# Optimization experiments

Measured on AMD Instinct MI355X. Metric: run time of the kernel, lower is better.

The kernel has to match this reference:

```python
import jax, jax.numpy as jnp
import numpy as np

DIM = 1536
DEPTH = 8
HEADS = 8
KV_HEADS = 1
GROUPS = HEADS // KV_HEADS
DQK = 128
DV = 192
DIM_PW = 128
POOL = 16
FF_INNER = int(DIM * 2.0)
SOFTCLAMP = 5.0
SCALE = 64 ** -0.5  # source uses default dim_head=64 for scale, not dim_head_qk
MAX_POS = 8192
EPS = float(jnp.finfo(jnp.float32).eps)


def rmsnorm(x, g):
    return x * jax.lax.rsqrt(jnp.mean(x * x, axis=-1, keepdims=True) + EPS) * g


def rotate_half(x):
    x1, x2 = jnp.split(x, 2, axis=-1)
    return jnp.concatenate([-x2, x1], axis=-1)


def apply_rope(pos, t):
    return t * jnp.cos(pos) + rotate_half(t) * jnp.sin(pos)


def rotary_emb(seq_len):
    nf = DQK // 2
    # torch.logspace(1, MAX_POS-nf+1, nf) = 10**linspace -> overflows to inf in fp32 (faithful)
    inv_freq = 1.0 / (jnp.arange(nf, dtype=jnp.float32) + 10.0 ** jnp.linspace(1.0, MAX_POS - nf + 1, nf, dtype=jnp.float32))
    freqs = jnp.arange(seq_len, dtype=jnp.float32)[:, None] * inv_freq[None, :]
    return jnp.concatenate([freqs, freqs], axis=-1)  # [n, DQK]


def softclamp(t, value=SOFTCLAMP):
    return jnp.tanh(t / value) * value


def attention(x, pairwise, rope, w_qkv, qg, kg, vg, bg, w_bias, w_out):
    b, n, _ = x.shape
    qkv = x @ w_qkv
    q, k, v = jnp.split(qkv, [HEADS * DQK, HEADS * DQK + DQK], axis=-1)
    # b n (g h d) -> b g h n d
    q = q.reshape(b, n, GROUPS, KV_HEADS, DQK).transpose(0, 2, 3, 1, 4)
    k = k.reshape(b, n, KV_HEADS, DQK).transpose(0, 2, 1, 3)
    v = v.reshape(b, n, KV_HEADS, DV).transpose(0, 2, 1, 3)
    q = rmsnorm(q, qg)
    k = rmsnorm(k, kg)
    v = rmsnorm(v, vg)
    q = q * SCALE
    q = apply_rope(rope, q)
    k = apply_rope(rope, k)
    sim = jnp.einsum('bghid,bhjd->bghij', q, k)
    # pairwise bias: RMSNorm -> GELU -> Linear(dim_pw, heads) -> b g h i j
    pb = jax.nn.gelu(rmsnorm(pairwise, bg), approximate=False) @ w_bias  # [b, i, j, heads]
    bi = pb.shape[1]
    bias = pb.reshape(b, bi, bi, GROUPS, KV_HEADS).transpose(0, 3, 4, 1, 2)
    bias = jnp.repeat(jnp.repeat(bias, POOL, axis=3), POOL, axis=4)  # expand to seq res
    sim = softclamp(sim + bias)
    attn = jax.nn.softmax(sim, axis=-1)
    out = jnp.einsum('bghij,bhjd->bghid', attn, v)
    out = out.transpose(0, 3, 1, 2, 4).reshape(b, n, GROUPS * KV_HEADS * DV)
    return out @ w_out


def tower(x, pairwise, w_qkv, q_gamma, k_gamma, v_gamma, bias_gamma, w_bias, w_out, attn_pre_gamma, ff_pre_gamma, w_ff1, b_ff1, w_ff2, b_ff2):
    rope = rotary_emb(x.shape[1])
    for d in range(DEPTH):
        xn = rmsnorm(x, attn_pre_gamma[d])
        x = x + attention(xn, pairwise, rope, w_qkv[d], q_gamma[d], k_gamma[d], v_gamma[d], bias_gamma[d], w_bias[d], w_out[d])
        xn = rmsnorm(x, ff_pre_gamma[d])
        x = x + (jax.nn.relu(xn @ w_ff1[d] + b_ff1[d]) @ w_ff2[d] + b_ff2[d])
    return x


def setup_inputs() -> dict:
    key = jax.random.key(0)
    ks = jax.random.split(key, 10)
    s = 0.02
    inp = {
        'x': jax.random.normal(ks[0], (2, 2048, DIM), jnp.float32),
        'pairwise': jax.random.normal(ks[1], (2, 128, 128, DIM_PW), jnp.float32),
        'w_qkv': jax.random.normal(ks[2], (DEPTH, DIM, HEADS * DQK + DQK + DV), jnp.float32) * s,
        'q_gamma': jnp.ones((DEPTH, DQK), jnp.float32),
        'k_gamma': jnp.ones((DEPTH, DQK), jnp.float32),
        'v_gamma': jnp.ones((DEPTH, DV), jnp.float32),
        'bias_gamma': jnp.ones((DEPTH, DIM_PW), jnp.float32),
        'w_bias': jax.random.normal(ks[3], (DEPTH, DIM_PW, HEADS), jnp.float32) * s,
        'w_out': jax.random.normal(ks[4], (DEPTH, DV * HEADS, DIM), jnp.float32) * s,
        'attn_pre_gamma': jnp.ones((DEPTH, DIM), jnp.float32),
        'ff_pre_gamma': jnp.ones((DEPTH, DIM), jnp.float32),
        'w_ff1': jax.random.normal(ks[5], (DEPTH, DIM, FF_INNER), jnp.float32) * s,
        'b_ff1': jnp.zeros((DEPTH, FF_INNER), jnp.float32),
        'w_ff2': jax.random.normal(ks[6], (DEPTH, FF_INNER, DIM), jnp.float32) * s,
        'b_ff2': jnp.zeros((DEPTH, DIM), jnp.float32),
    }
    return inp


def reference(x, pairwise, w_qkv, q_gamma, k_gamma, v_gamma, bias_gamma, w_bias, w_out, attn_pre_gamma, ff_pre_gamma, w_ff1, b_ff1, w_ff2, b_ff2):
    return tower(x, pairwise, w_qkv, q_gamma, k_gamma, v_gamma, bias_gamma, w_bias, w_out, attn_pre_gamma, ff_pre_gamma, w_ff1, b_ff1, w_ff2, b_ff2)
```

## Files before the change

### kernel.cpp

```cpp
#include <hip/hip_runtime.h>

typedef __bf16 bf16;
typedef float f32x4 __attribute__((ext_vector_type(4)));
typedef __bf16 bf16x8 __attribute__((ext_vector_type(8)));
typedef __bf16 bf16x4 __attribute__((ext_vector_type(4)));

#define EPSF 1.1920928955078125e-07f

#define GLOAD_LDS16(gsrc, ldst) \
  __builtin_amdgcn_global_load_lds((const __attribute__((address_space(1))) void*)(gsrc), \
                                   (__attribute__((address_space(3))) void*)(ldst), 16, 0, 0)

__device__ __forceinline__ float wave_reduce_sum(float v) {
#pragma unroll
  for (int m = 1; m < 64; m <<= 1) v += __shfl_xor(v, m, 64);
  return v;
}

__global__ __launch_bounds__(256) void wcast_t(const float* __restrict__ src,
                                               bf16* __restrict__ dst, int R, int C) {
  __shared__ float t[32][33];
  int z = blockIdx.z;
  const float* s = src + (size_t)z * R * C;
  bf16* d = dst + (size_t)z * R * C;
  int c0 = blockIdx.x * 32, r0 = blockIdx.y * 32;
  int tx = threadIdx.x, ty = threadIdx.y;
#pragma unroll
  for (int k = 0; k < 4; ++k)
    t[ty + k * 8][tx] = s[(size_t)(r0 + ty + k * 8) * C + c0 + tx];
  __syncthreads();
#pragma unroll
  for (int k = 0; k < 4; ++k)
    d[(size_t)(c0 + ty + k * 8) * R + r0 + tx] = (bf16)t[tx][ty + k * 8];
}

__global__ __launch_bounds__(256) void rmsnorm_k(const float* __restrict__ X,
                                                 const float* __restrict__ G,
                                                 bf16* __restrict__ O) {
  int row = blockIdx.x, tid = threadIdx.x, lane = tid & 63, w = tid >> 6;
  const float* x = X + (size_t)row * 1536;
  float v[6];
  float ss = 0.f;
#pragma unroll
  for (int k = 0; k < 6; ++k) { v[k] = x[tid + k * 256]; ss += v[k] * v[k]; }
  ss = wave_reduce_sum(ss);
  __shared__ float wsum[4];
  if (lane == 0) wsum[w] = ss;
  __syncthreads();
  ss = wsum[0] + wsum[1] + wsum[2] + wsum[3];
  float rs = rsqrtf(ss * (1.f / 1536.f) + EPSF);
  bf16* o = O + (size_t)row * 1536;
#pragma unroll
  for (int k = 0; k < 6; ++k) o[tid + k * 256] = (bf16)(v[k] * rs * G[tid + k * 256]);
}

template <int EPI>
__global__ __launch_bounds__(256, 3) void gemm_bt(const bf16* __restrict__ A,
                                                  const bf16* __restrict__ Bt,
                                                  float* __restrict__ Cf,
                                                  bf16* __restrict__ Cb,
                                                  const float* __restrict__ bias,
                                                  int M, int N, int K) {
  __shared__ __align__(16) char As[128 * 128];
  __shared__ __align__(16) char Bs[128 * 128];
  const int tid = threadIdx.x;
  const int lane = tid & 63, l15 = lane & 15, l4 = lane >> 4;
  const int w = tid >> 6;
  const int rm = blockIdx.y * 128;
  const int cn = blockIdx.x * 128;
  const int wm = (w >> 1) * 64, wn = (w & 1) * 64;
  f32x4 acc[4][4] = {};

  for (int kk = 0; kk < K; kk += 64) {
#pragma unroll
    for (int r = 0; r < 4; ++r) {
      uint32_t o = (uint32_t)(r * 256 + tid) * 16;
      uint32_t row = o >> 7;
      uint32_t kb = ((o >> 4) & 7) ^ (row & 7);
      const bf16* src = A + (size_t)(rm + (int)row) * K + kk + kb * 8;
      GLOAD_LDS16(src, As + (o & 0xFFFFFC00u));
    }
#pragma unroll
    for (int r = 0; r < 4; ++r) {
      uint32_t o = (uint32_t)(r * 256 + tid) * 16;
      uint32_t row = o >> 7;
      uint32_t kb = ((o >> 4) & 7) ^ (row & 7);
      int nrow = cn + (int)row;
      if (nrow >= N) nrow = N - 1;
      const bf16* src = Bt + (size_t)nrow * K + kk + kb * 8;
      GLOAD_LDS16(src, Bs + (o & 0xFFFFFC00u));
    }
    __syncthreads();
#pragma unroll
    for (int s = 0; s < 2; ++s) {
      bf16x8 a[4], b[4];
#pragma unroll
      for (int m = 0; m < 4; ++m) {
        uint32_t row = wm + m * 16 + l15;
        uint32_t kb = (uint32_t)(s * 4 + l4);
        a[m] = *(const bf16x8*)(As + row * 128 + (kb ^ (row & 7)) * 16);
      }
#pragma unroll
      for (int n = 0; n < 4; ++n) {
        uint32_t row = wn + n * 16 + l15;
        uint32_t kb = (uint32_t)(s * 4 + l4);
        b[n] = *(const bf16x8*)(Bs + row * 128 + (kb ^ (row & 7)) * 16);
      }
      __builtin_amdgcn_s_setprio(1);
#pragma unroll
      for (int m = 0; m < 4; ++m)
#pragma unroll
        for (int n = 0; n < 4; ++n)
          acc[m][n] = __builtin_amdgcn_mfma_f32_16x16x32_bf16(a[m], b[n], acc[m][n], 0, 0, 0);
      __builtin_amdgcn_s_setprio(0);
    }
    __syncthreads();
  }

#pragma unroll
  for (int m = 0; m < 4; ++m)
#pragma unroll
    for (int n = 0; n < 4; ++n)
#pragma unroll
      for (int r = 0; r < 4; ++r) {
        int row = rm + wm + m * 16 + l4 * 4 + r;
        int col = cn + wn + n * 16 + l15;
        if (col < N) {
          float v = acc[m][n][r];
          if constexpr (EPI == 0) {
            Cf[(size_t)row * N + col] = v;
          } else if constexpr (EPI == 2) {
            Cf[(size_t)row * N + col] += v;
          } else if constexpr (EPI == 3) {
            float tv = v + bias[col];
            Cb[(size_t)row * N + col] = (bf16)(tv > 0.f ? tv : 0.f);
          } else if constexpr (EPI == 4) {
            Cf[(size_t)row * N + col] += v + bias[col];
          }
        }
      }
}

__global__ void qkv_post(const float* __restrict__ qkv, const float* __restrict__ qg,
                         const float* __restrict__ kg, const float* __restrict__ vg,
                         bf16* __restrict__ Qo, bf16* __restrict__ Ko, bf16* __restrict__ Vo) {
  int t = blockIdx.x, seg = blockIdx.y, lane = threadIdx.x;
  int b = t >> 11, n = t & 2047;
  const float* base;
  const float* gamma;
  int len;
  if (seg < 8) { base = qkv + (size_t)t * 1344 + seg * 128; gamma = qg; len = 128; }
  else if (seg == 8) { base = qkv + (size_t)t * 1344 + 1024; gamma = kg; len = 128; }
  else { base = qkv + (size_t)t * 1344 + 1152; gamma = vg; len = 192; }
  float v0 = base[lane], v1 = base[lane + 64];
  float v2 = (len == 192) ? base[lane + 128] : 0.f;
  float ss = wave_reduce_sum(v0 * v0 + v1 * v1 + v2 * v2);
  float rs = rsqrtf(ss / (float)len + EPSF);
  float n0 = v0 * rs * gamma[lane];
  float n1 = v1 * rs * gamma[lane + 64];
  if (seg < 8) {
    n0 *= 0.125f; n1 *= 0.125f;
    if (lane == 0) {
      float th = 0.1f * (float)n;
      float c = cosf(th), s_ = sinf(th);
      float r0 = n0 * c - n1 * s_, r1 = n1 * c + n0 * s_;
      n0 = r0; n1 = r1;
    }
    bf16* q = Qo + ((size_t)((b * 8 + seg) * 2048 + n)) * 128;
    q[lane] = (bf16)n0; q[lane + 64] = (bf16)n1;
  } else if (seg == 8) {
    if (lane == 0) {
      float th = 0.1f * (float)n;
      float c = cosf(th), s_ = sinf(th);
      float r0 = n0 * c - n1 * s_, r1 = n1 * c + n0 * s_;
      n0 = r0; n1 = r1;
    }
    bf16* k = Ko + ((size_t)(b * 2048 + n)) * 128;
    k[lane] = (bf16)n0; k[lane + 64] = (bf16)n1;
  } else {
    float n2 = v2 * rs * vg[lane + 128];
    bf16* vp = Vo + ((size_t)(b * 2048 + n)) * 192;
    vp[lane] = (bf16)n0; vp[lane + 64] = (bf16)n1; vp[lane + 128] = (bf16)n2;
  }
}

__global__ __launch_bounds__(256) void vtrans(const bf16* __restrict__ V, bf16* __restrict__ Vt) {
  __shared__ bf16 t[32][33];
  int b = blockIdx.z;
  int j0 = blockIdx.x * 32, d0 = blockIdx.y * 32;
  int tx = threadIdx.x, ty = threadIdx.y;
#pragma unroll
  for (int k = 0; k < 4; ++k)
    t[ty + k * 8][tx] = V[((size_t)b * 2048 + j0 + ty + k * 8) * 192 + d0 + tx];
  __syncthreads();
#pragma unroll
  for (int k = 0; k < 4; ++k)
    Vt[((size_t)b * 192 + d0 + ty + k * 8) * 2048 + j0 + tx] = t[tx][ty + k * 8];
}

__global__ void bias_pw(const float* __restrict__ P, const float* __restrict__ g,
                        const float* __restrict__ Wb, float* __restrict__ Bout) {
  int j = blockIdx.x, i = blockIdx.y, b = blockIdx.z;
  int lane = threadIdx.x;
  const float* p = P + (((size_t)b * 128 + i) * 128 + j) * 128;
  float a0 = p[lane], a1 = p[lane + 64];
  float ss = wave_reduce_sum(a0 * a0 + a1 * a1);
  float rs = rsqrtf(ss * (1.f / 128.f) + EPSF);
  float x0 = a0 * rs * g[lane], x1 = a1 * rs * g[lane + 64];
  float g0 = 0.5f * x0 * (1.f + erff(x0 * 0.70710678118654752f));
  float g1 = 0.5f * x1 * (1.f + erff(x1 * 0.70710678118654752f));
  __shared__ float gs[128];
  gs[lane] = g0; gs[lane + 64] = g1;
  __syncthreads();
  int h = lane & 7;
  float acc = 0.f;
#pragma unroll
  for (int k = 0; k < 16; ++k) {
    int c = (lane >> 3) + k * 8;
    acc += gs[c] * Wb[c * 8 + h];
  }
  acc += __shfl_xor(acc, 8, 64);
  acc += __shfl_xor(acc, 16, 64);
  acc += __shfl_xor(acc, 32, 64);
  if (lane < 8) Bout[(((size_t)b * 8 + lane) * 128 + i) * 128 + j] = acc;
}

__global__ __launch_bounds__(256, 2) void attn_k(const bf16* __restrict__ Q,
                                                 const bf16* __restrict__ Kg,
                                                 const bf16* __restrict__ Vt,
                                                 const float* __restrict__ Bias,
                                                 bf16* __restrict__ O0, bf16* __restrict__ O1,
                                                 float* __restrict__ L0, float* __restrict__ L1) {
  __shared__ __align__(16) char Ks[64 * 256];
  __shared__ __align__(16) char Vs[192 * 128];
  __shared__ __align__(16) char Ps[128 * 128];
  __shared__ float BiasS[8 * 128];
  int tid = threadIdx.x, lane = tid & 63, w = tid >> 6;
  int it = blockIdx.x, g = blockIdx.y, bz = blockIdx.z;
  int b = bz >> 1, js = bz & 1;
  bf16* __restrict__ Op = js ? O1 : O0;
  float* __restrict__ Lp = js ? L1 : L0;
  int i0 = it * 128;
  int l15 = lane & 15, l4 = lane >> 4;

  bf16x8 qf[2][4];
#pragma unroll
  for (int m = 0; m < 2; ++m)
#pragma unroll
    for (int s = 0; s < 4; ++s)
      qf[m][s] = *(const bf16x8*)(Q + ((size_t)((b * 8 + g) * 2048 + i0 + w * 32 + m * 16 + l15)) * 128 + s * 32 + l4 * 8);

  {
    int r = tid >> 5, c = (tid & 31) * 4;
    *(float4*)&BiasS[r * 128 + c] =
        *(const float4*)(Bias + ((size_t)((b * 8 + g) * 128) + (i0 >> 4) + r) * 128 + c);
  }

  f32x4 accO[2][12] = {};
  float lacc[2] = {0.f, 0.f};

  for (int jt = js * 16; jt < js * 16 + 16; ++jt) {
    int j0 = jt * 64;
#pragma unroll
    for (int r = 0; r < 4; ++r) {
      uint32_t o = (uint32_t)(r * 256 + tid) * 16;
      uint32_t row = o >> 8;
      uint32_t kb = ((o >> 4) & 15) ^ (row & 15);
      const bf16* src = Kg + ((size_t)b * 2048 + j0 + (int)row) * 128 + kb * 8;
      GLOAD_LDS16(src, Ks + (o & 0xFFFFFC00u));
    }
#pragma unroll
    for (int r = 0; r < 6; ++r) {
      uint32_t o = (uint32_t)(r * 256 + tid) * 16;
      uint32_t dv = o >> 7;
      uint32_t kb = ((o >> 4) & 7) ^ (dv & 7);
      const bf16* src = Vt + ((size_t)b * 192 + dv) * 2048 + j0 + kb * 8;
      GLOAD_LDS16(src, Vs + (o & 0xFFFFFC00u));
    }
    __syncthreads();

    f32x4 accS[2][4] = {};
#pragma unroll
    for (int s = 0; s < 4; ++s) {
      bf16x8 kf[4];
#pragma unroll
      for (int n = 0; n < 4; ++n) {
        uint32_t row = n * 16 + l15;
        uint32_t kb = (uint32_t)(s * 4 + l4);
        kf[n] = *(const bf16x8*)(Ks + row * 256 + (kb ^ (row & 15)) * 16);
      }
      __builtin_amdgcn_s_setprio(1);
#pragma unroll
      for (int n = 0; n < 4; ++n)
#pragma unroll
        for (int m = 0; m < 2; ++m)
          accS[m][n] = __builtin_amdgcn_mfma_f32_16x16x32_bf16(kf[n], qf[m][s], accS[m][n], 0, 0, 0);
      __builtin_amdgcn_s_setprio(0);
    }

#pragma unroll
    for (int m = 0; m < 2; ++m) {
#pragma unroll
      for (int n = 0; n < 4; ++n) {
        float bia = BiasS[(w * 2 + m) * 128 + jt * 4 + n];
        bf16x4 pk;
#pragma unroll
        for (int r = 0; r < 4; ++r) {
          float sv = accS[m][n][r] + bia;
          float e1 = exp2f(0.57707801635558535f * sv);
          float th = 1.f - 2.f / (e1 + 1.f);
          float pv = exp2f(7.2134752044448170f * th);
          lacc[m] += pv;
          pk[r] = (bf16)pv;
        }
        uint32_t prow = (uint32_t)(w * 32 + m * 16 + l15);
        uint32_t byteo = prow * 128 + (uint32_t)(n * 16 + l4 * 4) * 2;
        byteo ^= (prow & 7) << 4;
        *(bf16x4*)(Ps + byteo) = pk;
      }
    }

#pragma unroll
    for (int s = 0; s < 2; ++s) {
      bf16x8 pa[2];
#pragma unroll
      for (int m = 0; m < 2; ++m) {
        uint32_t row = (uint32_t)(w * 32 + m * 16 + l15);
        uint32_t byteo = row * 128 + (uint32_t)(s * 64 + l4 * 16);
        byteo ^= (row & 7) << 4;
        pa[m] = *(const bf16x8*)(Ps + byteo);
      }
#pragma unroll
      for (int n = 0; n < 12; ++n) {
        uint32_t dvr = n * 16 + l15;
        uint32_t kb = (uint32_t)(s * 4 + l4);
        bf16x8 vf = *(const bf16x8*)(Vs + dvr * 128 + (kb ^ (dvr & 7)) * 16);
        __builtin_amdgcn_s_setprio(1);
#pragma unroll
        for (int m = 0; m < 2; ++m)
          accO[m][n] = __builtin_amdgcn_mfma_f32_16x16x32_bf16(vf, pa[m], accO[m][n], 0, 0, 0);
        __builtin_amdgcn_s_setprio(0);
      }
    }
    __syncthreads();
  }

#pragma unroll
  for (int m = 0; m < 2; ++m) {
    float l = lacc[m];
    l += __shfl_xor(l, 16, 64);
    l += __shfl_xor(l, 32, 64);
    lacc[m] = l;
  }
  if (l4 == 0) {
#pragma unroll
    for (int m = 0; m < 2; ++m)
      Lp[(size_t)(b * 8 + g) * 2048 + i0 + w * 32 + m * 16 + l15] = lacc[m];
  }

#pragma unroll
  for (int m = 0; m < 2; ++m) {
    int i = i0 + w * 32 + m * 16 + l15;
#pragma unroll
    for (int n = 0; n < 12; ++n) {
      bf16x4 ok;
#pragma unroll
      for (int r = 0; r < 4; ++r) ok[r] = (bf16)accO[m][n][r];
      int dv = n * 16 + l4 * 4;
      *(bf16x4*)(Op + ((size_t)(b * 8 + g) * 2048 + i) * 192 + dv) = ok;
    }
  }
}

__global__ __launch_bounds__(256) void attn_cmb(const bf16* __restrict__ O0,
                                                const bf16* __restrict__ O1,
                                                const float* __restrict__ L0,
                                                const float* __restrict__ L1,
                                                bf16* __restrict__ Out) {
  size_t e = ((size_t)blockIdx.x * 256u + threadIdx.x) * 8u;
  uint32_t dv = (uint32_t)(e % 192u);
  uint32_t rest = (uint32_t)(e / 192u);
  uint32_t i = rest & 2047u;
  uint32_t g = (rest >> 11) & 7u;
  uint32_t b = rest >> 14;
  bf16x8 a = *(const bf16x8*)(O0 + e);
  bf16x8 c = *(const bf16x8*)(O1 + e);
  float rl = 1.f / (L0[rest] + L1[rest]);
  bf16x8 t;
#pragma unroll
  for (int k = 0; k < 8; ++k) t[k] = (bf16)(((float)a[k] + (float)c[k]) * rl);
  *(bf16x8*)(Out + ((size_t)(b * 2048 + i)) * 1536 + g * 192 + dv) = t;
}

extern "C" void kernel_launch(void* const* d_in, const int* in_sizes, int n_in,
                              void* d_out, int out_size, void* d_ws, size_t ws_size,
                              hipStream_t stream) {
  (void)in_sizes; (void)n_in; (void)out_size;
  const float* x_in = (const float*)d_in[0];
  const float* pairwise = (const float*)d_in[1];
  const float* w_qkv = (const float*)d_in[2];
  const float* q_gamma = (const float*)d_in[3];
  const float* k_gamma = (const float*)d_in[4];
  const float* v_gamma = (const float*)d_in[5];
  const float* bias_gamma = (const float*)d_in[6];
  const float* w_bias = (const float*)d_in[7];
  const float* w_out = (const float*)d_in[8];
  const float* attn_pre = (const float*)d_in[9];
  const float* ff_pre = (const float*)d_in[10];
  const float* w_ff1 = (const float*)d_in[11];
  const float* b_ff1 = (const float*)d_in[12];
  const float* w_ff2 = (const float*)d_in[13];
  const float* b_ff2 = (const float*)d_in[14];

  char* p = (char*)d_ws;
  auto alloc = [&](size_t bytes) {
    char* r = p;
    p += (bytes + 255) & ~(size_t)255;
    return r;
  };
  bf16* wT_qkv = (bf16*)alloc(8ull * 1344 * 1536 * 2);
  bf16* wT_out = (bf16*)alloc(8ull * 1536 * 1536 * 2);
  bf16* wT_ff1 = (bf16*)alloc(8ull * 3072 * 1536 * 2);
  bf16* wT_ff2 = (bf16*)alloc(8ull * 1536 * 3072 * 2);
  float* x_ws = (float*)alloc(4096ull * 1536 * 4);
  bf16* xn = (bf16*)alloc(4096ull * 1536 * 2);
  float* qkvb = (float*)alloc(4096ull * 1344 * 4);
  bf16* qb = (bf16*)alloc(2ull * 8 * 2048 * 128 * 2);
  bf16* kb = (bf16*)alloc(2ull * 2048 * 128 * 2);
  bf16* vb = (bf16*)alloc(2ull * 2048 * 192 * 2);
  bf16* vtb = (bf16*)alloc(2ull * 192 * 2048 * 2);
  float* biasb = (float*)alloc(2ull * 8 * 128 * 128 * 4);
  bf16* attn_o = (bf16*)alloc(4096ull * 1536 * 2);
  bf16* hb = (bf16*)alloc(4096ull * 3072 * 2);
  bf16* op0 = (bf16*)alloc(2ull * 8 * 2048 * 192 * 2);
  bf16* op1 = (bf16*)alloc(2ull * 8 * 2048 * 192 * 2);
  float* lp0 = (float*)alloc(2ull * 8 * 2048 * 4);
  float* lp1 = (float*)alloc(2ull * 8 * 2048 * 4);
  if ((size_t)(p - (char*)d_ws) > ws_size) return;

  wcast_t<<<dim3(42, 48, 8), dim3(32, 8), 0, stream>>>(w_qkv, wT_qkv, 1536, 1344);
  wcast_t<<<dim3(48, 48, 8), dim3(32, 8), 0, stream>>>(w_out, wT_out, 1536, 1536);
  wcast_t<<<dim3(96, 48, 8), dim3(32, 8), 0, stream>>>(w_ff1, wT_ff1, 1536, 3072);
  wcast_t<<<dim3(48, 96, 8), dim3(32, 8), 0, stream>>>(w_ff2, wT_ff2, 3072, 1536);

  hipMemcpyAsync(x_ws, x_in, 4096ull * 1536 * 4, hipMemcpyDeviceToDevice, stream);

  for (int d = 0; d < 8; ++d) {
    const bf16* wq = wT_qkv + (size_t)d * 1344 * 1536;
    const bf16* wo = wT_out + (size_t)d * 1536 * 1536;
    const bf16* w1 = wT_ff1 + (size_t)d * 3072 * 1536;
    const bf16* w2 = wT_ff2 + (size_t)d * 1536 * 3072;

    rmsnorm_k<<<4096, 256, 0, stream>>>(x_ws, attn_pre + d * 1536, xn);
    gemm_bt<0><<<dim3(11, 32), 256, 0, stream>>>(xn, wq, qkvb, nullptr, nullptr, 4096, 1344, 1536);
    qkv_post<<<dim3(4096, 10), 64, 0, stream>>>(qkvb, q_gamma + d * 128, k_gamma + d * 128,
                                                v_gamma + d * 192, qb, kb, vb);
    vtrans<<<dim3(64, 6, 2), dim3(32, 8), 0, stream>>>(vb, vtb);
    bias_pw<<<dim3(128, 128, 2), 64, 0, stream>>>(pairwise, bias_gamma + d * 128,
                                                  w_bias + d * 128 * 8, biasb);
    attn_k<<<dim3(16, 8, 4), 256, 0, stream>>>(qb, kb, vtb, biasb, op0, op1, lp0, lp1);
    attn_cmb<<<3072, 256, 0, stream>>>(op0, op1, lp0, lp1, attn_o);
    gemm_bt<2><<<dim3(12, 32), 256, 0, stream>>>(attn_o, wo, x_ws, nullptr, nullptr, 4096, 1536, 1536);
    rmsnorm_k<<<4096, 256, 0, stream>>>(x_ws, ff_pre + d * 1536, xn);
    gemm_bt<3><<<dim3(24, 32), 256, 0, stream>>>(xn, w1, nullptr, hb, b_ff1 + d * 3072, 4096, 3072, 1536);
    gemm_bt<4><<<dim3(12, 32), 256, 0, stream>>>(hb, w2, x_ws, nullptr, b_ff2 + d * 1536, 4096, 1536, 3072);
  }

  hipMemcpyAsync(d_out, x_ws, 4096ull * 1536 * 4, hipMemcpyDeviceToDevice, stream);
}
```

Baseline: 2.876 ms.

## Split-K GEMMs with atomic accumulation, XCD block swizzle, and cheaper softclamp math

Three GEMMs now split K in two across blockIdx.z and accumulate with float atomicAdd into the output. The QKV output is zeroed first with a memset. Block IDs are remapped so consecutive tiles go to the same XCD, which targets L2 reuse. The attention kernel pre-scales the bias and rewrites the tanh-then-exp softclamp as one FMA, an exp2, a hardware reciprocal and an exp2; attn_cmb also uses the hardware reciprocal. Split-K aims to fill 256 CUs with the small grids, but it adds atomic traffic, an extra memset, and non-deterministic summation order.

```diff
diff --git a/kernel.cpp b/kernel.cpp
--- a/kernel.cpp
+++ b/kernel.cpp
@@ -54,7 +54,7 @@
   for (int k = 0; k < 6; ++k) o[tid + k * 256] = (bf16)(v[k] * rs * G[tid + k * 256]);
 }
 
-template <int EPI>
+template <int EPI, int SPLIT>
 __global__ __launch_bounds__(256, 3) void gemm_bt(const bf16* __restrict__ A,
                                                   const bf16* __restrict__ Bt,
                                                   float* __restrict__ Cf,
@@ -66,12 +66,21 @@
   const int tid = threadIdx.x;
   const int lane = tid & 63, l15 = lane & 15, l4 = lane >> 4;
   const int w = tid >> 6;
-  const int rm = blockIdx.y * 128;
-  const int cn = blockIdx.x * 128;
+  const int nwg = gridDim.x * gridDim.y;
+  const int bid = blockIdx.y * gridDim.x + blockIdx.x;
+  const int cpx = nwg >> 3;
+  const int swz = (bid & 7) * cpx + (bid >> 3);
+  const int rm = (swz / gridDim.x) * 128;
+  const int cn = (swz % gridDim.x) * 128;
   const int wm = (w >> 1) * 64, wn = (w & 1) * 64;
+  int kbeg = 0, kend = K;
+  if constexpr (SPLIT == 2) {
+    kbeg = blockIdx.z * (K >> 1);
+    kend = kbeg + (K >> 1);
+  }
   f32x4 acc[4][4] = {};
 
-  for (int kk = 0; kk < K; kk += 64) {
+  for (int kk = kbeg; kk < kend; kk += 64) {
 #pragma unroll
     for (int r = 0; r < 4; ++r) {
       uint32_t o = (uint32_t)(r * 256 + tid) * 16;
@@ -127,15 +136,21 @@
         int col = cn + wn + n * 16 + l15;
         if (col < N) {
           float v = acc[m][n][r];
+          size_t idx = (size_t)row * N + col;
           if constexpr (EPI == 0) {
-            Cf[(size_t)row * N + col] = v;
+            if constexpr (SPLIT > 1) atomicAdd(&Cf[idx], v);
+            else Cf[idx] = v;
           } else if constexpr (EPI == 2) {
-            Cf[(size_t)row * N + col] += v;
+            if constexpr (SPLIT > 1) atomicAdd(&Cf[idx], v);
+            else Cf[idx] += v;
           } else if constexpr (EPI == 3) {
             float tv = v + bias[col];
-            Cb[(size_t)row * N + col] = (bf16)(tv > 0.f ? tv : 0.f);
+            Cb[idx] = (bf16)(tv > 0.f ? tv : 0.f);
           } else if constexpr (EPI == 4) {
-            Cf[(size_t)row * N + col] += v + bias[col];
+            float add = v;
+            if (SPLIT == 1 || blockIdx.z == 0) add += bias[col];
+            if constexpr (SPLIT > 1) atomicAdd(&Cf[idx], add);
+            else Cf[idx] += add;
           }
         }
       }
@@ -252,8 +267,10 @@
 
   {
     int r = tid >> 5, c = (tid & 31) * 4;
-    *(float4*)&BiasS[r * 128 + c] =
-        *(const float4*)(Bias + ((size_t)((b * 8 + g) * 128) + (i0 >> 4) + r) * 128 + c);
+    float4 bv = *(const float4*)(Bias + ((size_t)((b * 8 + g) * 128) + (i0 >> 4) + r) * 128 + c);
+    bv.x *= 0.57707801635558535f; bv.y *= 0.57707801635558535f;
+    bv.z *= 0.57707801635558535f; bv.w *= 0.57707801635558535f;
+    *(float4*)&BiasS[r * 128 + c] = bv;
   }
 
   f32x4 accO[2][12] = {};
@@ -302,14 +319,14 @@
     for (int m = 0; m < 2; ++m) {
 #pragma unroll
       for (int n = 0; n < 4; ++n) {
-        float bia = BiasS[(w * 2 + m) * 128 + jt * 4 + n];
+        float biaS = BiasS[(w * 2 + m) * 128 + jt * 4 + n];
         bf16x4 pk;
 #pragma unroll
         for (int r = 0; r < 4; ++r) {
-          float sv = accS[m][n][r] + bia;
-          float e1 = exp2f(0.57707801635558535f * sv);
-          float th = 1.f - 2.f / (e1 + 1.f);
-          float pv = exp2f(7.2134752044448170f * th);
+          float t1 = __builtin_fmaf(0.57707801635558535f, accS[m][n][r], biaS);
+          float e1 = exp2f(t1);
+          float rr = __builtin_amdgcn_rcpf(e1 + 1.0f);
+          float pv = exp2f(-14.426950408889634f * rr);
           lacc[m] += pv;
           pk[r] = (bf16)pv;
         }
@@ -385,7 +402,7 @@
   uint32_t b = rest >> 14;
   bf16x8 a = *(const bf16x8*)(O0 + e);
   bf16x8 c = *(const bf16x8*)(O1 + e);
-  float rl = 1.f / (L0[rest] + L1[rest]);
+  float rl = __builtin_amdgcn_rcpf(L0[rest] + L1[rest]);
   bf16x8 t;
 #pragma unroll
   for (int k = 0; k < 8; ++k) t[k] = (bf16)(((float)a[k] + (float)c[k]) * rl);
@@ -452,7 +469,8 @@
     const bf16* w2 = wT_ff2 + (size_t)d * 1536 * 3072;
 
     rmsnorm_k<<<4096, 256, 0, stream>>>(x_ws, attn_pre + d * 1536, xn);
-    gemm_bt<0><<<dim3(11, 32), 256, 0, stream>>>(xn, wq, qkvb, nullptr, nullptr, 4096, 1344, 1536);
+    hipMemsetAsync(qkvb, 0, 4096ull * 1344 * 4, stream);
+    gemm_bt<0, 2><<<dim3(11, 32, 2), 256, 0, stream>>>(xn, wq, qkvb, nullptr, nullptr, 4096, 1344, 1536);
     qkv_post<<<dim3(4096, 10), 64, 0, stream>>>(qkvb, q_gamma + d * 128, k_gamma + d * 128,
                                                 v_gamma + d * 192, qb, kb, vb);
     vtrans<<<dim3(64, 6, 2), dim3(32, 8), 0, stream>>>(vb, vtb);
@@ -460,10 +478,10 @@
                                                   w_bias + d * 128 * 8, biasb);
     attn_k<<<dim3(16, 8, 4), 256, 0, stream>>>(qb, kb, vtb, biasb, op0, op1, lp0, lp1);
     attn_cmb<<<3072, 256, 0, stream>>>(op0, op1, lp0, lp1, attn_o);
-    gemm_bt<2><<<dim3(12, 32), 256, 0, stream>>>(attn_o, wo, x_ws, nullptr, nullptr, 4096, 1536, 1536);
+    gemm_bt<2, 2><<<dim3(12, 32, 2), 256, 0, stream>>>(attn_o, wo, x_ws, nullptr, nullptr, 4096, 1536, 1536);
     rmsnorm_k<<<4096, 256, 0, stream>>>(x_ws, ff_pre + d * 1536, xn);
-    gemm_bt<3><<<dim3(24, 32), 256, 0, stream>>>(xn, w1, nullptr, hb, b_ff1 + d * 3072, 4096, 3072, 1536);
-    gemm_bt<4><<<dim3(12, 32), 256, 0, stream>>>(hb, w2, x_ws, nullptr, b_ff2 + d * 1536, 4096, 1536, 3072);
+    gemm_bt<3, 1><<<dim3(24, 32), 256, 0, stream>>>(xn, w1, nullptr, hb, b_ff1 + d * 3072, 4096, 3072, 1536);
+    gemm_bt<4, 2><<<dim3(12, 32, 2), 256, 0, stream>>>(hb, w2, x_ws, nullptr, b_ff2 + d * 1536, 4096, 1536, 3072);
   }
 
   hipMemcpyAsync(d_out, x_ws, 4096ull * 1536 * 4, hipMemcpyDeviceToDevice, stream);
```

After: 2.988 ms. 1.04x slower.
